# Kernel optimization log

Measured on AMD Instinct MI355X. Metric: run time of the kernel, lower is better.

The kernel has to match this reference:

```python
import math
import jax, jax.numpy as jnp
import numpy as np

B, N, M, D, H = 1, 768, 768, 128, 8
DH = D // H
CHUNK = 256  # coord_chunk_M default


def _ln(x, g, b):
    mu = jnp.mean(x, -1, keepdims=True)
    var = jnp.mean((x - mu) ** 2, -1, keepdims=True)
    return (x - mu) * jax.lax.rsqrt(var + 1e-5) * g + b


def setup_inputs() -> dict:
    key = jax.random.key(0)
    ks = jax.random.split(key, 32)
    def rn(i, shape, s=0.02):
        return jax.random.normal(ks[i], shape, jnp.float32) * s
    z = lambda *s: jnp.zeros(s, jnp.float32)
    o = lambda *s: jnp.ones(s, jnp.float32)
    return {
        "h_q": jax.random.normal(ks[0], (B, N, D), jnp.float32),
        "x_q": jax.random.normal(ks[1], (B, N, 3), jnp.float32),
        "h_r": jax.random.normal(ks[2], (B, M, D), jnp.float32),
        "x_r": jax.random.normal(ks[3], (B, M, 3), jnp.float32),
        "mask_q": jnp.ones((B, N), bool),
        "mask_r": jnp.ones((B, M), bool),
        "Wq": rn(4, (D, D)), "bqp": z(D),
        "Wk": rn(5, (D, D)), "bkp": z(D),
        "Wv": rn(6, (D, D)), "bvp": z(D),
        "Wo": rn(7, (D, D)), "bop": z(D),
        "g_nq": o(D), "b_nq": z(D),
        "g_nr": o(D), "b_nr": z(D),
        "g_ff": o(D), "b_ff": z(D),
        "W1": rn(8, (4 * D, D)), "b1": z(4 * D),
        "W2": rn(9, (D, 4 * D)), "b2": z(D),
        "k_null": rn(10, (H, DH)),
        "v_null": rn(11, (H, DH)),
        "b_null": jnp.full((H,), -1.0, jnp.float32),
        "We1": rn(12, (D, 2 * D + 1)), "be1": z(D),
        "We2": rn(13, (D, D)), "be2": z(D),
        "Ws": rn(14, (1, D), 0.01),
    }


def reference(h_q, x_q, h_r, x_r, mask_q, mask_r,
              Wq, bqp, Wk, bkp, Wv, bvp, Wo, bop,
              g_nq, b_nq, g_nr, b_nr, g_ff, b_ff,
              W1, b1, W2, b2, k_null, v_null, b_null,
              We1, be1, We2, be2, Ws):
    inv = 1.0 / math.sqrt(DH)
    qh = _ln(h_q, g_nq, b_nq)
    q = (qh @ Wq.T + bqp).reshape(B, N, H, DH).transpose(0, 2, 1, 3)   # bhnd
    rh = _ln(h_r, g_nr, b_nr)
    k = (rh @ Wk.T + bkp).reshape(B, M, H, DH).transpose(0, 2, 1, 3)   # bhmd
    v = (h_r @ Wv.T + bvp).reshape(B, M, H, DH).transpose(0, 2, 1, 3)  # v from raw h_r (as in source)

    pair = mask_q[:, None, :, None] & mask_r[:, None, None, :]          # b1nm
    neg = jnp.finfo(jnp.float32).min
    logits = jnp.einsum('bhnd,bhmd->bhnm', q, k) * inv
    logits = jnp.where(pair, logits, neg)
    lnull = jnp.einsum('bhnd,hd->bhn', q, k_null) * inv + b_null[None, :, None]

    mx = jnp.max(logits, -1, keepdims=True)
    lse_real = (mx + jnp.log(jnp.sum(jnp.exp(logits - mx), -1, keepdims=True) + 1e-9))[..., 0]
    lse_all = jnp.logaddexp(lse_real, lnull)                            # bhn
    a_real = jnp.exp(logits - lse_all[..., None])                       # bhnm
    a_null = jnp.exp(lnull - lse_all)                                   # bhn

    msg = jnp.einsum('bhnm,bhmd->bhnd', a_real, v) + a_null[..., None] * v_null[None, :, None, :]
    h_msg = msg.transpose(0, 2, 1, 3).reshape(B, N, D)
    h_out = h_q + h_msg @ Wo.T + bop
    t = _ln(h_out, g_ff, b_ff)
    h_out = h_out + jax.nn.silu(t @ W1.T + b1) @ W2.T + b2

    # coordinate update
    gate = jnp.mean(jnp.clip(jnp.sum(a_real, -1), 0.0, 1.0), axis=1)[..., None]  # b n 1
    a_s = jnp.mean(a_real, axis=1)                                               # b n m
    qh_new = _ln(h_out, g_nq, b_nq)
    nC = M // CHUNK
    xr_c = x_r.reshape(B, nC, CHUNK, 3).transpose(1, 0, 2, 3)
    rh_c = rh.reshape(B, nC, CHUNK, D).transpose(1, 0, 2, 3)
    mr_c = mask_r.reshape(B, nC, CHUNK).transpose(1, 0, 2)
    a_c = a_s.reshape(B, N, nC, CHUNK).transpose(2, 0, 1, 3)

    def step(dx, inp):
        xr, rhb, mr, a = inp
        diff = x_q[:, :, None, :] - xr[:, None, :, :]                   # b n c 3
        radial = jnp.sum(diff * diff, -1, keepdims=True)
        dirn = diff * jax.lax.rsqrt(radial + 1e-8)
        qb = jnp.broadcast_to(qh_new[:, :, None, :], (B, N, CHUNK, D))
        rb = jnp.broadcast_to(rhb[:, None, :, :], (B, N, CHUNK, D))
        edge = jnp.concatenate([qb, rb, radial], -1)                    # b n c 2D+1
        s = (jax.nn.silu(jax.nn.silu(edge @ We1.T + be1) @ We2.T + be2) @ Ws.T)[..., 0]
        valid = mask_q[:, :, None] & mr[:, None, :]
        sw = jnp.where(valid, s * a, 0.0)
        return dx + jnp.sum(dirn * sw[..., None], axis=2), None

    dx, _ = jax.lax.scan(step, jnp.zeros_like(x_q), (xr_c, rh_c, mr_c, a_c))
    x_out = x_q + dx * gate
    return (h_out, x_out)
```

## Files before the change

### kernel.cpp

```cpp
#include <hip/hip_runtime.h>
#include <hip/hip_bf16.h>
#include <math.h>

#define N_ 768
#define M_ 768
#define D_ 128
#define H_ 8
#define DH_ 16
#define FF_ 512
#define CH_ 4
#define CM_ 192

typedef float f32x4 __attribute__((ext_vector_type(4)));
typedef short bf16x8 __attribute__((ext_vector_type(8)));
typedef unsigned short u16x8 __attribute__((ext_vector_type(8)));

__device__ __forceinline__ float siluf(float x) {
    return x * __builtin_amdgcn_rcpf(1.0f + __expf(-x));
}

__device__ __forceinline__ unsigned short f2bf(float x) {
    unsigned int u = __float_as_uint(x);
    unsigned int r = (u + 0x7fffu + ((u >> 16) & 1u)) >> 16;
    return (unsigned short)r;
}

__device__ __forceinline__ short f2bf_rn(float x) {
    __hip_bfloat16 b = __float2bfloat16(x);
    return (short)*reinterpret_cast<unsigned short*>(&b);
}

__device__ __forceinline__ float bf2f(unsigned short u) {
    return __uint_as_float(((unsigned int)u) << 16);
}

__global__ __launch_bounds__(64) void k_ln2(const float* __restrict__ h_q,
                                            const float* __restrict__ h_r,
                                            const float* __restrict__ g_nq, const float* __restrict__ b_nq,
                                            const float* __restrict__ g_nr, const float* __restrict__ b_nr,
                                            float* __restrict__ qh, float* __restrict__ rh,
                                            const float* __restrict__ We2, unsigned short* __restrict__ We2b,
                                            const float* __restrict__ We1, float* __restrict__ We1a) {
    int row = blockIdx.x, lane = threadIdx.x;
    const float *src, *g, *b; float* dst;
    if (row < N_) { src = h_q + row * D_; g = g_nq; b = b_nq; dst = qh + row * D_; }
    else { src = h_r + (row - N_) * D_; g = g_nr; b = b_nr; dst = rh + (row - N_) * D_; }
    float x0 = src[lane], x1 = src[lane + 64];
    float s = x0 + x1;
#pragma unroll
    for (int o = 32; o > 0; o >>= 1) s += __shfl_xor(s, o);
    float mu = s * (1.f / 128.f);
    float d0 = x0 - mu, d1 = x1 - mu;
    float v2 = d0 * d0 + d1 * d1;
#pragma unroll
    for (int o = 32; o > 0; o >>= 1) v2 += __shfl_xor(v2, o);
    float inv = rsqrtf(v2 * (1.f / 128.f) + 1e-5f);
    dst[lane] = d0 * inv * g[lane] + b[lane];
    dst[lane + 64] = d1 * inv * g[lane + 64] + b[lane + 64];
    if (row < D_) {
        We2b[row * D_ + lane] = f2bf(We2[row * D_ + lane]);
        We2b[row * D_ + lane + 64] = f2bf(We2[row * D_ + lane + 64]);
    }
    if (row <= 256) {
        We1a[row * D_ + lane] = We1[lane * 257 + row];
        We1a[row * D_ + lane + 64] = We1[(lane + 64) * 257 + row];
    }
}

__global__ __launch_bounds__(128) void k_qkv(const float* __restrict__ qh,
                                             const float* __restrict__ rh,
                                             const float* __restrict__ h_r,
                                             const float* __restrict__ Wq, const float* __restrict__ bq,
                                             const float* __restrict__ Wk, const float* __restrict__ bk,
                                             const float* __restrict__ Wv, const float* __restrict__ bv,
                                             float* __restrict__ q,
                                             unsigned short* __restrict__ kb,
                                             unsigned short* __restrict__ vb) {
    int r0 = blockIdx.x * 8, which = blockIdx.y, j = threadIdx.x;
    const float* in; const float* W; const float* b;
    if (which == 0) { in = qh; W = Wq; b = bq; }
    else if (which == 1) { in = rh; W = Wk; b = bk; }
    else { in = h_r; W = Wv; b = bv; }
    __shared__ float xs[8][D_];
    for (int i = j; i < 8 * D_; i += 128) xs[i >> 7][i & 127] = in[r0 * D_ + i];
    __syncthreads();
    const float4* Wr = (const float4*)(W + j * D_);
    float acc[8] = {0, 0, 0, 0, 0, 0, 0, 0};
    for (int i = 0; i < 32; i++) {
        float4 w = Wr[i];
#pragma unroll
        for (int r = 0; r < 8; r++) {
            float4 x = ((const float4*)xs[r])[i];
            acc[r] += w.x * x.x + w.y * x.y + w.z * x.z + w.w * x.w;
        }
    }
    float bb = b[j];
    if (which == 0) {
#pragma unroll
        for (int r = 0; r < 8; r++) q[(r0 + r) * D_ + j] = acc[r] + bb;
    } else {
        unsigned short* outb = (which == 1) ? kb : vb;
#pragma unroll
        for (int r = 0; r < 8; r++) outb[(r0 + r) * D_ + j] = (unsigned short)f2bf_rn(acc[r] + bb);
    }
}

__global__ __launch_bounds__(512) void k_attn(const float* __restrict__ q,
                                              const unsigned short* __restrict__ kb,
                                              const unsigned short* __restrict__ vb,
                                              const float* __restrict__ k_null,
                                              const float* __restrict__ v_null,
                                              const float* __restrict__ b_null,
                                              float* __restrict__ a_s,
                                              float* __restrict__ gate,
                                              float* __restrict__ msg) {
    int n = blockIdx.x, t = threadIdx.x;
    int h = t >> 6, lane = t & 63;
    __shared__ float ew[H_][M_];
    __shared__ float gate_p[H_];
    const float inv = 0.25f;

    float qr[DH_];
    const float* qp = q + n * D_ + h * DH_;
#pragma unroll
    for (int d = 0; d < DH_; d++) qr[d] = qp[d];

    float ll[12];
    float lmax = -3.4e38f;
#pragma unroll
    for (int i = 0; i < 12; i++) {
        int m = lane + 64 * i;
        const unsigned short* kp = kb + m * D_ + h * DH_;
        u16x8 k0 = *(const u16x8*)kp;
        u16x8 k1 = *(const u16x8*)(kp + 8);
        float acc = 0.f;
#pragma unroll
        for (int d = 0; d < 8; d++) acc += qr[d] * bf2f(k0[d]);
#pragma unroll
        for (int d = 0; d < 8; d++) acc += qr[d + 8] * bf2f(k1[d]);
        acc *= inv;
        ll[i] = acc;
        lmax = fmaxf(lmax, acc);
    }
#pragma unroll
    for (int o = 32; o > 0; o >>= 1) lmax = fmaxf(lmax, __shfl_xor(lmax, o));
    float es = 0.f;
#pragma unroll
    for (int i = 0; i < 12; i++) es += __expf(ll[i] - lmax);
#pragma unroll
    for (int o = 32; o > 0; o >>= 1) es += __shfl_xor(es, o);

    float lnull;
    {
        const float* kp = k_null + h * DH_;
        float acc = 0.f;
#pragma unroll
        for (int d = 0; d < DH_; d++) acc += qr[d] * kp[d];
        lnull = acc * inv + b_null[h];
    }
    float lse_real = lmax + __logf(es + 1e-9f);
    float m2 = fmaxf(lse_real, lnull);
    float lse_all = m2 + __logf(__expf(lse_real - m2) + __expf(lnull - m2));
    float a_null = __expf(lnull - lse_all);
    if (lane == 0) gate_p[h] = fminf(1.f, __expf(lse_real - lse_all));

#pragma unroll
    for (int i = 0; i < 12; i++) ew[h][lane + 64 * i] = __expf(ll[i] - lse_all);

    int d = lane & 15, sub = lane >> 4;
    float p = 0.f;
    const f32x4* ewv = (const f32x4*)&ew[h][0];
#pragma unroll 4
    for (int i = 0; i < 48; i++) {
        int m0 = i * 16 + sub * 4;
        f32x4 a4 = ewv[i * 4 + sub];
        const unsigned short* vp = vb + m0 * D_ + h * DH_ + d;
        p += a4[0] * bf2f(vp[0]);
        p += a4[1] * bf2f(vp[D_]);
        p += a4[2] * bf2f(vp[2 * D_]);
        p += a4[3] * bf2f(vp[3 * D_]);
    }
    p += __shfl_xor(p, 16);
    p += __shfl_xor(p, 32);
    if (lane < 16) msg[n * D_ + h * DH_ + lane] = p + a_null * v_null[h * DH_ + lane];

    __syncthreads();
    for (int m = t; m < M_; m += 512) {
        float s = 0.f;
#pragma unroll
        for (int hh = 0; hh < H_; hh++) s += ew[hh][m];
        a_s[n * M_ + m] = s * 0.125f;
    }
    if (t == 0) {
        float s = 0.f;
#pragma unroll
        for (int hh = 0; hh < H_; hh++) s += gate_p[hh];
        gate[n] = s * 0.125f;
    }
}

__global__ __launch_bounds__(256) void k_mlp(const float* __restrict__ h_q,
                                             const float* __restrict__ msg,
                                             const float* __restrict__ Wo, const float* __restrict__ bop,
                                             const float* __restrict__ g_ff, const float* __restrict__ b_ff,
                                             const float* __restrict__ W1, const float* __restrict__ b1,
                                             const float* __restrict__ W2, const float* __restrict__ b2,
                                             const float* __restrict__ g_nq, const float* __restrict__ b_nq,
                                             float* __restrict__ h_out, float* __restrict__ qh_new) {
    int r0 = blockIdx.x * 8;
    int t = threadIdx.x;
    __shared__ float xs[8][D_];
    __shared__ float hm[8][D_];
    __shared__ float tl[8][D_];
    __shared__ float ffh[8][FF_];
    for (int i = t; i < 8 * D_; i += 256) xs[i >> 7][i & 127] = msg[r0 * D_ + i];
    __syncthreads();
    {
        int g = t >> 7, j = t & 127;
        float acc[4] = {0, 0, 0, 0};
        const float4* Wr = (const float4*)(Wo + j * D_);
        for (int i = 0; i < 32; i++) {
            float4 w = Wr[i];
#pragma unroll
            for (int r = 0; r < 4; r++) {
                float4 x = ((const float4*)xs[4 * g + r])[i];
                acc[r] += w.x * x.x + w.y * x.y + w.z * x.z + w.w * x.w;
            }
        }
        float bb = bop[j];
#pragma unroll
        for (int r = 0; r < 4; r++)
            hm[4 * g + r][j] = h_q[(r0 + 4 * g + r) * D_ + j] + acc[r] + bb;
    }
    __syncthreads();
    {
        int r = t >> 5, l = t & 31;
        float v0 = hm[r][l], v1 = hm[r][l + 32], v2 = hm[r][l + 64], v3 = hm[r][l + 96];
        float s = v0 + v1 + v2 + v3;
#pragma unroll
        for (int o = 1; o < 32; o <<= 1) s += __shfl_xor(s, o);
        float mu = s * (1.f / 128.f);
        float d0 = v0 - mu, d1 = v1 - mu, d2 = v2 - mu, d3 = v3 - mu;
        float vv = d0 * d0 + d1 * d1 + d2 * d2 + d3 * d3;
#pragma unroll
        for (int o = 1; o < 32; o <<= 1) vv += __shfl_xor(vv, o);
        float inv = rsqrtf(vv * (1.f / 128.f) + 1e-5f);
        tl[r][l] = d0 * inv * g_ff[l] + b_ff[l];
        tl[r][l + 32] = d1 * inv * g_ff[l + 32] + b_ff[l + 32];
        tl[r][l + 64] = d2 * inv * g_ff[l + 64] + b_ff[l + 64];
        tl[r][l + 96] = d3 * inv * g_ff[l + 96] + b_ff[l + 96];
    }
    __syncthreads();
    {
        int j0 = t, j1 = t + 256;
        float a0[8] = {0}, a1[8] = {0};
        const float4* Wa = (const float4*)(W1 + j0 * D_);
        const float4* Wb = (const float4*)(W1 + j1 * D_);
        for (int i = 0; i < 32; i++) {
            float4 wa = Wa[i], wb = Wb[i];
#pragma unroll
            for (int r = 0; r < 8; r++) {
                float4 x = ((const float4*)tl[r])[i];
                a0[r] += wa.x * x.x + wa.y * x.y + wa.z * x.z + wa.w * x.w;
                a1[r] += wb.x * x.x + wb.y * x.y + wb.z * x.z + wb.w * x.w;
            }
        }
        float bb0 = b1[j0], bb1 = b1[j1];
#pragma unroll
        for (int r = 0; r < 8; r++) {
            ffh[r][j0] = siluf(a0[r] + bb0);
            ffh[r][j1] = siluf(a1[r] + bb1);
        }
    }
    __syncthreads();
    {
        int g = t >> 7, j = t & 127;
        float acc[4] = {0, 0, 0, 0};
        const float4* Wr = (const float4*)(W2 + j * FF_);
        for (int i = 0; i < 128; i++) {
            float4 w = Wr[i];
#pragma unroll
            for (int r = 0; r < 4; r++) {
                float4 x = ((const float4*)ffh[4 * g + r])[i];
                acc[r] += w.x * x.x + w.y * x.y + w.z * x.z + w.w * x.w;
            }
        }
        float bb = b2[j];
#pragma unroll
        for (int r = 0; r < 4; r++) {
            float vv = hm[4 * g + r][j] + acc[r] + bb;
            h_out[(r0 + 4 * g + r) * D_ + j] = vv;
            hm[4 * g + r][j] = vv;
        }
    }
    __syncthreads();
    {
        int r = t >> 5, l = t & 31;
        float v0 = hm[r][l], v1 = hm[r][l + 32], v2 = hm[r][l + 64], v3 = hm[r][l + 96];
        float s = v0 + v1 + v2 + v3;
#pragma unroll
        for (int o = 1; o < 32; o <<= 1) s += __shfl_xor(s, o);
        float mu = s * (1.f / 128.f);
        float d0 = v0 - mu, d1 = v1 - mu, d2 = v2 - mu, d3 = v3 - mu;
        float vv = d0 * d0 + d1 * d1 + d2 * d2 + d3 * d3;
#pragma unroll
        for (int o = 1; o < 32; o <<= 1) vv += __shfl_xor(vv, o);
        float inv = rsqrtf(vv * (1.f / 128.f) + 1e-5f);
        int rr = (r0 + r) * D_;
        qh_new[rr + l] = d0 * inv * g_nq[l] + b_nq[l];
        qh_new[rr + l + 32] = d1 * inv * g_nq[l + 32] + b_nq[l + 32];
        qh_new[rr + l + 64] = d2 * inv * g_nq[l + 64] + b_nq[l + 64];
        qh_new[rr + l + 96] = d3 * inv * g_nq[l + 96] + b_nq[l + 96];
    }
}

__global__ __launch_bounds__(256) void k_pre(const float* __restrict__ qh_new,
                                             const float* __restrict__ rh,
                                             const float* __restrict__ We1a,
                                             const float* __restrict__ be1,
                                             float* __restrict__ Aq,
                                             float* __restrict__ Br) {
    int bb = blockIdx.x;
    int half = bb >= 48;
    int r0 = (bb - half * 48) * 16;
    int off = half * 128;
    int t = threadIdx.x;
    int r = t >> 4, jg = t & 15;
    __shared__ float xs[16][D_];
    const float* in = (half ? rh : qh_new) + r0 * D_;
    for (int i = t; i < 16 * D_; i += 256) xs[i >> 7][i & 127] = in[i];
    __syncthreads();
    float acc[8] = {0};
    const float* xr = xs[r];
    for (int i = 0; i < 128; i++) {
        float x = xr[i];
        const float4 w0 = *(const float4*)(We1a + (off + i) * D_ + jg * 8);
        const float4 w1 = *(const float4*)(We1a + (off + i) * D_ + jg * 8 + 4);
        acc[0] += w0.x * x; acc[1] += w0.y * x; acc[2] += w0.z * x; acc[3] += w0.w * x;
        acc[4] += w1.x * x; acc[5] += w1.y * x; acc[6] += w1.z * x; acc[7] += w1.w * x;
    }
    float* out = (half ? Br : Aq) + (r0 + r) * D_ + jg * 8;
    if (half) {
        const float4 e0 = *(const float4*)(be1 + jg * 8);
        const float4 e1 = *(const float4*)(be1 + jg * 8 + 4);
        acc[0] += e0.x; acc[1] += e0.y; acc[2] += e0.z; acc[3] += e0.w;
        acc[4] += e1.x; acc[5] += e1.y; acc[6] += e1.z; acc[7] += e1.w;
    }
    *(float4*)(out) = make_float4(acc[0], acc[1], acc[2], acc[3]);
    *(float4*)(out + 4) = make_float4(acc[4], acc[5], acc[6], acc[7]);
}

__global__ __launch_bounds__(256, 4) void k_pair(const float* __restrict__ x_q,
                                                 const float* __restrict__ x_r,
                                                 const float* __restrict__ Aq,
                                                 const float* __restrict__ Br,
                                                 const float* __restrict__ w1r,
                                                 const float* __restrict__ be2,
                                                 const float* __restrict__ Ws,
                                                 const unsigned short* __restrict__ We2b,
                                                 const float* __restrict__ a_s,
                                                 float* __restrict__ dxp) {
    int n = blockIdx.x;
    int chunk = blockIdx.y;
    int cm = chunk * CM_;
    int t = threadIdx.x;
    int w = t >> 6;
    int lane = t & 63;
    int col = lane & 15;
    int kg = lane >> 4;

    __shared__ bf16x8 af_st[4][4][64];
    __shared__ float part_s[4][64];
    __shared__ float xr_l[CM_ * 3];
    __shared__ float as_l[CM_];
    __shared__ float Aq_l[D_];
    __shared__ float w1r_l[D_];
    __shared__ float2 bw_l[D_];

    for (int i = t; i < CM_ * 3; i += 256) xr_l[i] = x_r[cm * 3 + i];
    if (t < CM_) as_l[t] = a_s[n * M_ + cm + t];
    if (t < D_) {
        Aq_l[t] = Aq[n * D_ + t];
        w1r_l[t] = w1r[t];
        bw_l[t] = make_float2(be2[t], Ws[t]);
    }
    __syncthreads();

    bf16x8 bfr[2][4];
#pragma unroll
    for (int q2 = 0; q2 < 2; q2++)
#pragma unroll
        for (int kt = 0; kt < 4; kt++)
            bfr[q2][kt] = *reinterpret_cast<const bf16x8*>(We2b + ((w * 2 + q2) * 16 + col) * D_ + kt * 32 + kg * 8);

    float2 bwv[2][4];
#pragma unroll
    for (int q2 = 0; q2 < 2; q2++)
#pragma unroll
        for (int r = 0; r < 4; r++)
            bwv[q2][r] = bw_l[(w * 2 + q2) * 16 + kg * 4 + r];

    float xq0 = x_q[n * 3 + 0], xq1 = x_q[n * 3 + 1], xq2 = x_q[n * 3 + 2];
    float dxa = 0.f, dya = 0.f, dza = 0.f;

    for (int it = 0; it < CM_ / 64; it++) {
        int mb = it * 64;
        {
            int pm = mb + w * 16 + col;
            float d0 = xq0 - xr_l[pm * 3], d1 = xq1 - xr_l[pm * 3 + 1], d2 = xq2 - xr_l[pm * 3 + 2];
            float radial = d0 * d0 + d1 * d1 + d2 * d2;
#pragma unroll
            for (int kt = 0; kt < 4; kt++) {
                int ob = kt * 32 + kg * 8;
                const float4* brp = reinterpret_cast<const float4*>(Br + (cm + pm) * D_ + ob);
                float4 b0 = brp[0], b1 = brp[1];
                const float4 a0 = *(const float4*)(Aq_l + ob), a1 = *(const float4*)(Aq_l + ob + 4);
                const float4 w0 = *(const float4*)(w1r_l + ob), w1 = *(const float4*)(w1r_l + ob + 4);
                bf16x8 af;
                af[0] = f2bf_rn(siluf(a0.x + b0.x + radial * w0.x));
                af[1] = f2bf_rn(siluf(a0.y + b0.y + radial * w0.y));
                af[2] = f2bf_rn(siluf(a0.z + b0.z + radial * w0.z));
                af[3] = f2bf_rn(siluf(a0.w + b0.w + radial * w0.w));
                af[4] = f2bf_rn(siluf(a1.x + b1.x + radial * w1.x));
                af[5] = f2bf_rn(siluf(a1.y + b1.y + radial * w1.y));
                af[6] = f2bf_rn(siluf(a1.z + b1.z + radial * w1.z));
                af[7] = f2bf_rn(siluf(a1.w + b1.w + radial * w1.w));
                af_st[w][kt][lane] = af;
            }
        }
        __syncthreads();
        float sg[4];
#pragma unroll
        for (int g = 0; g < 4; g++) {
            f32x4 acc0 = {0.f, 0.f, 0.f, 0.f}, acc1 = {0.f, 0.f, 0.f, 0.f};
#pragma unroll
            for (int kt = 0; kt < 4; kt++) {
                bf16x8 a = af_st[g][kt][lane];
                acc0 = __builtin_amdgcn_mfma_f32_16x16x32_bf16(bfr[0][kt], a, acc0, 0, 0, 0);
                acc1 = __builtin_amdgcn_mfma_f32_16x16x32_bf16(bfr[1][kt], a, acc1, 0, 0, 0);
            }
            float sv = 0.f;
#pragma unroll
            for (int r = 0; r < 4; r++) {
                sv += siluf(acc0[r] + bwv[0][r].x) * bwv[0][r].y;
                sv += siluf(acc1[r] + bwv[1][r].x) * bwv[1][r].y;
            }
            sv += __shfl_xor(sv, 16);
            sv += __shfl_xor(sv, 32);
            sg[g] = sv;
        }
        if (lane < 16) {
#pragma unroll
            for (int g = 0; g < 4; g++) part_s[w][g * 16 + lane] = sg[g];
        }
        __syncthreads();
        if (t < 64) {
            float s = part_s[0][t] + part_s[1][t] + part_s[2][t] + part_s[3][t];
            int m2 = mb + t;
            float sw = s * as_l[m2];
            float e0 = xq0 - xr_l[m2 * 3], e1 = xq1 - xr_l[m2 * 3 + 1], e2 = xq2 - xr_l[m2 * 3 + 2];
            float ir = rsqrtf(e0 * e0 + e1 * e1 + e2 * e2 + 1e-8f);
            dxa += e0 * ir * sw;
            dya += e1 * ir * sw;
            dza += e2 * ir * sw;
        }
    }
    if (t < 64) {
#pragma unroll
        for (int o = 1; o < 64; o <<= 1) {
            dxa += __shfl_xor(dxa, o);
            dya += __shfl_xor(dya, o);
            dza += __shfl_xor(dza, o);
        }
        if (t == 0) {
            float* o = dxp + (chunk * N_ + n) * 3;
            o[0] = dxa; o[1] = dya; o[2] = dza;
        }
    }
}

__global__ __launch_bounds__(256) void k_fin(const float* __restrict__ x_q,
                                             const float* __restrict__ dxp,
                                             const float* __restrict__ gate,
                                             float* __restrict__ x_out) {
    int i = blockIdx.x * 256 + threadIdx.x;
    if (i >= N_ * 3) return;
    int n = i / 3;
    float s = 0.f;
#pragma unroll
    for (int ch = 0; ch < CH_; ch++) s += dxp[(ch * N_ + n) * 3 + (i - n * 3)];
    x_out[i] = x_q[i] + s * gate[n];
}

extern "C" void kernel_launch(void* const* d_in, const int* in_sizes, int n_in,
                              void* d_out, int out_size, void* d_ws, size_t ws_size,
                              hipStream_t stream) {
    const float* h_q   = (const float*)d_in[0];
    const float* x_q   = (const float*)d_in[1];
    const float* h_r   = (const float*)d_in[2];
    const float* x_r   = (const float*)d_in[3];
    const float* Wq    = (const float*)d_in[6];
    const float* bqp   = (const float*)d_in[7];
    const float* Wk    = (const float*)d_in[8];
    const float* bkp   = (const float*)d_in[9];
    const float* Wv    = (const float*)d_in[10];
    const float* bvp   = (const float*)d_in[11];
    const float* Wo    = (const float*)d_in[12];
    const float* bop   = (const float*)d_in[13];
    const float* g_nq  = (const float*)d_in[14];
    const float* b_nq  = (const float*)d_in[15];
    const float* g_nr  = (const float*)d_in[16];
    const float* b_nr  = (const float*)d_in[17];
    const float* g_ff  = (const float*)d_in[18];
    const float* b_ff  = (const float*)d_in[19];
    const float* W1    = (const float*)d_in[20];
    const float* b1    = (const float*)d_in[21];
    const float* W2    = (const float*)d_in[22];
    const float* b2    = (const float*)d_in[23];
    const float* k_null= (const float*)d_in[24];
    const float* v_null= (const float*)d_in[25];
    const float* b_null= (const float*)d_in[26];
    const float* We1   = (const float*)d_in[27];
    const float* be1   = (const float*)d_in[28];
    const float* We2   = (const float*)d_in[29];
    const float* be2   = (const float*)d_in[30];
    const float* Ws    = (const float*)d_in[31];

    float* ws     = (float*)d_ws;
    float* qh     = ws;
    float* rh     = qh + N_ * D_;
    float* q      = rh + M_ * D_;
    unsigned short* kb = (unsigned short*)(q + N_ * D_);
    unsigned short* vb = kb + M_ * D_;
    float* a_s    = (float*)(vb + M_ * D_);
    float* gate   = a_s + N_ * M_;
    float* msg    = gate + N_;
    float* qh_new = msg + N_ * D_;
    float* Aq     = qh_new + N_ * D_;
    float* Br     = Aq + N_ * D_;
    float* We1a   = Br + M_ * D_;
    float* dxp    = We1a + 257 * D_;
    unsigned short* We2b = (unsigned short*)(dxp + CH_ * N_ * 3);
    float* w1r    = We1a + 256 * D_;

    float* h_out = (float*)d_out;
    float* x_out = h_out + N_ * D_;

    k_ln2<<<N_ + M_, 64, 0, stream>>>(h_q, h_r, g_nq, b_nq, g_nr, b_nr, qh, rh, We2, We2b, We1, We1a);
    k_qkv<<<dim3(96, 3), 128, 0, stream>>>(qh, rh, h_r, Wq, bqp, Wk, bkp, Wv, bvp, q, kb, vb);
    k_attn<<<N_, 512, 0, stream>>>(q, kb, vb, k_null, v_null, b_null, a_s, gate, msg);
    k_mlp<<<96, 256, 0, stream>>>(h_q, msg, Wo, bop, g_ff, b_ff, W1, b1, W2, b2, g_nq, b_nq, h_out, qh_new);
    k_pre<<<96, 256, 0, stream>>>(qh_new, rh, We1a, be1, Aq, Br);
    k_pair<<<dim3(N_, CH_), 256, 0, stream>>>(x_q, x_r, Aq, Br, w1r, be2, Ws, We2b, a_s, dxp);
    k_fin<<<9, 256, 0, stream>>>(x_q, dxp, gate, x_out);
}
```

Before: 163.0 us.

## Halve rows per block in mlp/pre kernels and drop cross-wave reduction in pair kernel

k_mlp and k_pre now process half as many rows per block and launch twice the blocks, so more of the GPU's compute units have work. In k_pair, each lane now applies its partial score directly to the coordinate update instead of reducing scores through shared memory. This removes one barrier and the single-wave tail per iteration and frees LDS, with the occupancy hint raised to 6. Per-wave results are combined once at the end via a small shared array. In exchange, weight reads per row are amortised less and each lane does more redundant geometry work.

Result: slower. 252.3 us (+54.8%).

```diff
diff --git a/kernel.cpp b/kernel.cpp
--- a/kernel.cpp
+++ b/kernel.cpp
@@ -207,59 +207,57 @@
                                              const float* __restrict__ W2, const float* __restrict__ b2,
                                              const float* __restrict__ g_nq, const float* __restrict__ b_nq,
                                              float* __restrict__ h_out, float* __restrict__ qh_new) {
-    int r0 = blockIdx.x * 8;
+    int r0 = blockIdx.x * 4;
     int t = threadIdx.x;
-    __shared__ float xs[8][D_];
-    __shared__ float hm[8][D_];
-    __shared__ float tl[8][D_];
-    __shared__ float ffh[8][FF_];
-    for (int i = t; i < 8 * D_; i += 256) xs[i >> 7][i & 127] = msg[r0 * D_ + i];
+    __shared__ float xs[4][D_];
+    __shared__ float hm[4][D_];
+    __shared__ float tl[4][D_];
+    __shared__ float ffh[4][FF_];
+    for (int i = t; i < 4 * D_; i += 256) xs[i >> 7][i & 127] = msg[r0 * D_ + i];
     __syncthreads();
     {
         int g = t >> 7, j = t & 127;
-        float acc[4] = {0, 0, 0, 0};
+        float acc[2] = {0, 0};
         const float4* Wr = (const float4*)(Wo + j * D_);
         for (int i = 0; i < 32; i++) {
             float4 w = Wr[i];
 #pragma unroll
-            for (int r = 0; r < 4; r++) {
-                float4 x = ((const float4*)xs[4 * g + r])[i];
+            for (int r = 0; r < 2; r++) {
+                float4 x = ((const float4*)xs[2 * g + r])[i];
                 acc[r] += w.x * x.x + w.y * x.y + w.z * x.z + w.w * x.w;
             }
         }
         float bb = bop[j];
 #pragma unroll
-        for (int r = 0; r < 4; r++)
-            hm[4 * g + r][j] = h_q[(r0 + 4 * g + r) * D_ + j] + acc[r] + bb;
+        for (int r = 0; r < 2; r++)
+            hm[2 * g + r][j] = h_q[(r0 + 2 * g + r) * D_ + j] + acc[r] + bb;
     }
     __syncthreads();
     {
-        int r = t >> 5, l = t & 31;
-        float v0 = hm[r][l], v1 = hm[r][l + 32], v2 = hm[r][l + 64], v3 = hm[r][l + 96];
-        float s = v0 + v1 + v2 + v3;
-#pragma unroll
-        for (int o = 1; o < 32; o <<= 1) s += __shfl_xor(s, o);
+        int r = t >> 6, l = t & 63;
+        float v0 = hm[r][l], v1 = hm[r][l + 64];
+        float s = v0 + v1;
+#pragma unroll
+        for (int o = 32; o > 0; o >>= 1) s += __shfl_xor(s, o);
         float mu = s * (1.f / 128.f);
-        float d0 = v0 - mu, d1 = v1 - mu, d2 = v2 - mu, d3 = v3 - mu;
-        float vv = d0 * d0 + d1 * d1 + d2 * d2 + d3 * d3;
-#pragma unroll
-        for (int o = 1; o < 32; o <<= 1) vv += __shfl_xor(vv, o);
+        float d0 = v0 - mu, d1 = v1 - mu;
+        float vv = d0 * d0 + d1 * d1;
+#pragma unroll
+        for (int o = 32; o > 0; o >>= 1) vv += __shfl_xor(vv, o);
         float inv = rsqrtf(vv * (1.f / 128.f) + 1e-5f);
         tl[r][l] = d0 * inv * g_ff[l] + b_ff[l];
-        tl[r][l + 32] = d1 * inv * g_ff[l + 32] + b_ff[l + 32];
-        tl[r][l + 64] = d2 * inv * g_ff[l + 64] + b_ff[l + 64];
-        tl[r][l + 96] = d3 * inv * g_ff[l + 96] + b_ff[l + 96];
+        tl[r][l + 64] = d1 * inv * g_ff[l + 64] + b_ff[l + 64];
     }
     __syncthreads();
     {
         int j0 = t, j1 = t + 256;
-        float a0[8] = {0}, a1[8] = {0};
+        float a0[4] = {0}, a1[4] = {0};
         const float4* Wa = (const float4*)(W1 + j0 * D_);
         const float4* Wb = (const float4*)(W1 + j1 * D_);
         for (int i = 0; i < 32; i++) {
             float4 wa = Wa[i], wb = Wb[i];
 #pragma unroll
-            for (int r = 0; r < 8; r++) {
+            for (int r = 0; r < 4; r++) {
                 float4 x = ((const float4*)tl[r])[i];
                 a0[r] += wa.x * x.x + wa.y * x.y + wa.z * x.z + wa.w * x.w;
                 a1[r] += wb.x * x.x + wb.y * x.y + wb.z * x.z + wb.w * x.w;
@@ -267,7 +265,7 @@
         }
         float bb0 = b1[j0], bb1 = b1[j1];
 #pragma unroll
-        for (int r = 0; r < 8; r++) {
+        for (int r = 0; r < 4; r++) {
             ffh[r][j0] = siluf(a0[r] + bb0);
             ffh[r][j1] = siluf(a1[r] + bb1);
         }
@@ -275,42 +273,40 @@
     __syncthreads();
     {
         int g = t >> 7, j = t & 127;
-        float acc[4] = {0, 0, 0, 0};
+        float acc[2] = {0, 0};
         const float4* Wr = (const float4*)(W2 + j * FF_);
         for (int i = 0; i < 128; i++) {
             float4 w = Wr[i];
 #pragma unroll
-            for (int r = 0; r < 4; r++) {
-                float4 x = ((const float4*)ffh[4 * g + r])[i];
+            for (int r = 0; r < 2; r++) {
+                float4 x = ((const float4*)ffh[2 * g + r])[i];
                 acc[r] += w.x * x.x + w.y * x.y + w.z * x.z + w.w * x.w;
             }
         }
         float bb = b2[j];
 #pragma unroll
-        for (int r = 0; r < 4; r++) {
-            float vv = hm[4 * g + r][j] + acc[r] + bb;
-            h_out[(r0 + 4 * g + r) * D_ + j] = vv;
-            hm[4 * g + r][j] = vv;
+        for (int r = 0; r < 2; r++) {
+            float vv = hm[2 * g + r][j] + acc[r] + bb;
+            h_out[(r0 + 2 * g + r) * D_ + j] = vv;
+            hm[2 * g + r][j] = vv;
         }
     }
     __syncthreads();
     {
-        int r = t >> 5, l = t & 31;
-        float v0 = hm[r][l], v1 = hm[r][l + 32], v2 = hm[r][l + 64], v3 = hm[r][l + 96];
-        float s = v0 + v1 + v2 + v3;
-#pragma unroll
-        for (int o = 1; o < 32; o <<= 1) s += __shfl_xor(s, o);
+        int r = t >> 6, l = t & 63;
+        float v0 = hm[r][l], v1 = hm[r][l + 64];
+        float s = v0 + v1;
+#pragma unroll
+        for (int o = 32; o > 0; o >>= 1) s += __shfl_xor(s, o);
         float mu = s * (1.f / 128.f);
-        float d0 = v0 - mu, d1 = v1 - mu, d2 = v2 - mu, d3 = v3 - mu;
-        float vv = d0 * d0 + d1 * d1 + d2 * d2 + d3 * d3;
-#pragma unroll
-        for (int o = 1; o < 32; o <<= 1) vv += __shfl_xor(vv, o);
+        float d0 = v0 - mu, d1 = v1 - mu;
+        float vv = d0 * d0 + d1 * d1;
+#pragma unroll
+        for (int o = 32; o > 0; o >>= 1) vv += __shfl_xor(vv, o);
         float inv = rsqrtf(vv * (1.f / 128.f) + 1e-5f);
         int rr = (r0 + r) * D_;
         qh_new[rr + l] = d0 * inv * g_nq[l] + b_nq[l];
-        qh_new[rr + l + 32] = d1 * inv * g_nq[l + 32] + b_nq[l + 32];
-        qh_new[rr + l + 64] = d2 * inv * g_nq[l + 64] + b_nq[l + 64];
-        qh_new[rr + l + 96] = d3 * inv * g_nq[l + 96] + b_nq[l + 96];
+        qh_new[rr + l + 64] = d1 * inv * g_nq[l + 64] + b_nq[l + 64];
     }
 }
 
@@ -321,36 +317,31 @@
                                              float* __restrict__ Aq,
                                              float* __restrict__ Br) {
     int bb = blockIdx.x;
-    int half = bb >= 48;
-    int r0 = (bb - half * 48) * 16;
+    int half = bb >= 96;
+    int r0 = (bb - half * 96) * 8;
     int off = half * 128;
     int t = threadIdx.x;
-    int r = t >> 4, jg = t & 15;
-    __shared__ float xs[16][D_];
+    int r = t >> 5, jg = t & 31;
+    __shared__ float xs[8][D_];
     const float* in = (half ? rh : qh_new) + r0 * D_;
-    for (int i = t; i < 16 * D_; i += 256) xs[i >> 7][i & 127] = in[i];
-    __syncthreads();
-    float acc[8] = {0};
+    for (int i = t; i < 8 * D_; i += 256) xs[i >> 7][i & 127] = in[i];
+    __syncthreads();
+    float acc[4] = {0, 0, 0, 0};
     const float* xr = xs[r];
     for (int i = 0; i < 128; i++) {
         float x = xr[i];
-        const float4 w0 = *(const float4*)(We1a + (off + i) * D_ + jg * 8);
-        const float4 w1 = *(const float4*)(We1a + (off + i) * D_ + jg * 8 + 4);
+        const float4 w0 = *(const float4*)(We1a + (off + i) * D_ + jg * 4);
         acc[0] += w0.x * x; acc[1] += w0.y * x; acc[2] += w0.z * x; acc[3] += w0.w * x;
-        acc[4] += w1.x * x; acc[5] += w1.y * x; acc[6] += w1.z * x; acc[7] += w1.w * x;
-    }
-    float* out = (half ? Br : Aq) + (r0 + r) * D_ + jg * 8;
+    }
     if (half) {
-        const float4 e0 = *(const float4*)(be1 + jg * 8);
-        const float4 e1 = *(const float4*)(be1 + jg * 8 + 4);
+        const float4 e0 = *(const float4*)(be1 + jg * 4);
         acc[0] += e0.x; acc[1] += e0.y; acc[2] += e0.z; acc[3] += e0.w;
-        acc[4] += e1.x; acc[5] += e1.y; acc[6] += e1.z; acc[7] += e1.w;
-    }
+    }
+    float* out = (half ? Br : Aq) + (r0 + r) * D_ + jg * 4;
     *(float4*)(out) = make_float4(acc[0], acc[1], acc[2], acc[3]);
-    *(float4*)(out + 4) = make_float4(acc[4], acc[5], acc[6], acc[7]);
-}
-
-__global__ __launch_bounds__(256, 4) void k_pair(const float* __restrict__ x_q,
+}
+
+__global__ __launch_bounds__(256, 6) void k_pair(const float* __restrict__ x_q,
                                                  const float* __restrict__ x_r,
                                                  const float* __restrict__ Aq,
                                                  const float* __restrict__ Br,
@@ -370,19 +361,15 @@
     int kg = lane >> 4;
 
     __shared__ bf16x8 af_st[4][4][64];
-    __shared__ float part_s[4][64];
     __shared__ float xr_l[CM_ * 3];
-    __shared__ float as_l[CM_];
     __shared__ float Aq_l[D_];
     __shared__ float w1r_l[D_];
-    __shared__ float2 bw_l[D_];
+    __shared__ float dxw[4][3];
 
     for (int i = t; i < CM_ * 3; i += 256) xr_l[i] = x_r[cm * 3 + i];
-    if (t < CM_) as_l[t] = a_s[n * M_ + cm + t];
     if (t < D_) {
         Aq_l[t] = Aq[n * D_ + t];
         w1r_l[t] = w1r[t];
-        bw_l[t] = make_float2(be2[t], Ws[t]);
     }
     __syncthreads();
 
@@ -397,11 +384,14 @@
 #pragma unroll
     for (int q2 = 0; q2 < 2; q2++)
 #pragma unroll
-        for (int r = 0; r < 4; r++)
-            bwv[q2][r] = bw_l[(w * 2 + q2) * 16 + kg * 4 + r];
+        for (int r = 0; r < 4; r++) {
+            int p = (w * 2 + q2) * 16 + kg * 4 + r;
+            bwv[q2][r] = make_float2(be2[p], Ws[p]);
+        }
 
     float xq0 = x_q[n * 3 + 0], xq1 = x_q[n * 3 + 1], xq2 = x_q[n * 3 + 2];
     float dxa = 0.f, dya = 0.f, dza = 0.f;
+    const float* asg = a_s + n * M_ + cm;
 
     for (int it = 0; it < CM_ / 64; it++) {
         int mb = it * 64;
@@ -429,7 +419,6 @@
             }
         }
         __syncthreads();
-        float sg[4];
 #pragma unroll
         for (int g = 0; g < 4; g++) {
             f32x4 acc0 = {0.f, 0.f, 0.f, 0.f}, acc1 = {0.f, 0.f, 0.f, 0.f};
@@ -445,37 +434,29 @@
                 sv += siluf(acc0[r] + bwv[0][r].x) * bwv[0][r].y;
                 sv += siluf(acc1[r] + bwv[1][r].x) * bwv[1][r].y;
             }
-            sv += __shfl_xor(sv, 16);
-            sv += __shfl_xor(sv, 32);
-            sg[g] = sv;
-        }
-        if (lane < 16) {
-#pragma unroll
-            for (int g = 0; g < 4; g++) part_s[w][g * 16 + lane] = sg[g];
-        }
-        __syncthreads();
-        if (t < 64) {
-            float s = part_s[0][t] + part_s[1][t] + part_s[2][t] + part_s[3][t];
-            int m2 = mb + t;
-            float sw = s * as_l[m2];
+            int m2 = mb + g * 16 + col;
+            float sw = sv * asg[m2];
             float e0 = xq0 - xr_l[m2 * 3], e1 = xq1 - xr_l[m2 * 3 + 1], e2 = xq2 - xr_l[m2 * 3 + 2];
             float ir = rsqrtf(e0 * e0 + e1 * e1 + e2 * e2 + 1e-8f);
             dxa += e0 * ir * sw;
             dya += e1 * ir * sw;
             dza += e2 * ir * sw;
         }
-    }
-    if (t < 64) {
-#pragma unroll
-        for (int o = 1; o < 64; o <<= 1) {
-            dxa += __shfl_xor(dxa, o);
-            dya += __shfl_xor(dya, o);
-            dza += __shfl_xor(dza, o);
-        }
-        if (t == 0) {
-            float* o = dxp + (chunk * N_ + n) * 3;
-            o[0] = dxa; o[1] = dya; o[2] = dza;
-        }
+        __syncthreads();
+    }
+#pragma unroll
+    for (int o = 1; o < 64; o <<= 1) {
+        dxa += __shfl_xor(dxa, o);
+        dya += __shfl_xor(dya, o);
+        dza += __shfl_xor(dza, o);
+    }
+    if (lane == 0) { dxw[w][0] = dxa; dxw[w][1] = dya; dxw[w][2] = dza; }
+    __syncthreads();
+    if (t == 0) {
+        float* o = dxp + (chunk * N_ + n) * 3;
+        o[0] = dxw[0][0] + dxw[1][0] + dxw[2][0] + dxw[3][0];
+        o[1] = dxw[0][1] + dxw[1][1] + dxw[2][1] + dxw[3][1];
+        o[2] = dxw[0][2] + dxw[1][2] + dxw[2][2] + dxw[3][2];
     }
 }
 
@@ -549,8 +530,8 @@
     k_ln2<<<N_ + M_, 64, 0, stream>>>(h_q, h_r, g_nq, b_nq, g_nr, b_nr, qh, rh, We2, We2b, We1, We1a);
     k_qkv<<<dim3(96, 3), 128, 0, stream>>>(qh, rh, h_r, Wq, bqp, Wk, bkp, Wv, bvp, q, kb, vb);
     k_attn<<<N_, 512, 0, stream>>>(q, kb, vb, k_null, v_null, b_null, a_s, gate, msg);
-    k_mlp<<<96, 256, 0, stream>>>(h_q, msg, Wo, bop, g_ff, b_ff, W1, b1, W2, b2, g_nq, b_nq, h_out, qh_new);
-    k_pre<<<96, 256, 0, stream>>>(qh_new, rh, We1a, be1, Aq, Br);
+    k_mlp<<<192, 256, 0, stream>>>(h_q, msg, Wo, bop, g_ff, b_ff, W1, b1, W2, b2, g_nq, b_nq, h_out, qh_new);
+    k_pre<<<192, 256, 0, stream>>>(qh_new, rh, We1a, be1, Aq, Br);
     k_pair<<<dim3(N_, CH_), 256, 0, stream>>>(x_q, x_r, Aq, Br, w1r, be2, Ws, We2b, a_s, dxp);
     k_fin<<<9, 256, 0, stream>>>(x_q, dxp, gate, x_out);
 }
```
